# Kernel tuning notes

Measured on AMD Instinct MI355X. Metric: run time of the kernel, lower is better.

## Reference

```python
import jax, jax.numpy as jnp
import numpy as np

SR = 16000
NFFT = 512
NFILT = 64
FRAME_LEN = 400    # 0.025 * 16000
FRAME_STEP = 160   # 0.010 * 16000
NUM_FRAMES = 50000


def _mel_filterbanks():
    # python_speech_features get_filterbanks(nfilt=64, nfft=512, sr=16000, lowfreq=0, highfreq=sr/2)
    def hz2mel(hz):
        return 2595.0 * np.log10(1.0 + hz / 700.0)

    def mel2hz(m):
        return 700.0 * (10.0 ** (m / 2595.0) - 1.0)

    highfreq = SR / 2.0
    melpts = np.linspace(hz2mel(0.0), hz2mel(highfreq), NFILT + 2)
    bins = np.floor((NFFT + 1) * mel2hz(melpts) / SR)
    fb = np.zeros((NFILT, NFFT // 2 + 1), dtype=np.float64)
    for j in range(NFILT):
        for i in range(int(bins[j]), int(bins[j + 1])):
            fb[j, i] = (i - bins[j]) / (bins[j + 1] - bins[j])
        for i in range(int(bins[j + 1]), int(bins[j + 2])):
            fb[j, i] = (bins[j + 2] - i) / (bins[j + 2] - bins[j + 1])
    return fb.T.astype(np.float32)  # (257, nfilt) == filters.T in the original


def setup_inputs() -> dict:
    key = jax.random.key(0)
    audio_len = FRAME_LEN + (NUM_FRAMES - 1) * FRAME_STEP  # 8_000_240 -> exactly 50000 frames, zero pad
    x = jax.random.normal(key, (1, audio_len), dtype=jnp.float32)
    filters = jnp.asarray(_mel_filterbanks())
    return {"x": x, "filters": filters}


def reference(x, filters):
    # pre-emphasis
    x = jnp.concatenate([x[:, :1], x[:, 1:] - 0.97 * x[:, :-1]], axis=1)
    audio_len = x.shape[1]
    num_frames = (audio_len - FRAME_LEN) // FRAME_STEP + 1
    # vectorized framing (replaces the per-frame python slice/stack loop)
    idx = jnp.arange(num_frames)[:, None] * FRAME_STEP + jnp.arange(FRAME_LEN)[None, :]
    windowed = x[:, idx]                                     # (B, F, frame_len)
    r = jnp.fft.rfft(windowed, n=NFFT, axis=2)               # (B, F, nfft//2+1)
    power = (jnp.real(r) ** 2 + jnp.imag(r) ** 2) * (1.0 / NFFT)
    feat = jnp.einsum('bfk,kn->bfn', power, filters) + 1e-30  # (B, F, nfilt)
    # per-frame normalization over (batch, filters), matching reduce_mean/K.std on feat[:, i, :]
    m = jnp.mean(feat, axis=(0, 2), keepdims=True)
    s = jnp.std(feat, axis=(0, 2), keepdims=True)
    feat = (feat - m) / s
    return feat[..., None]                                   # (1, F, nfilt, 1)
```

## Files before the change

kernel.cpp:

```cpp
#include <hip/hip_runtime.h>
#include <math.h>

#define NFILT 64
#define FRAME_LEN 400
#define FRAME_STEP 160
#define WMAX 24
#define WSTRIDE 25
#define WAVES 4
#define NBLOCKS 1563
#define PWBINS 280

__global__ __launch_bounds__(256) void fbank_kernel(const float* __restrict__ x,
                                                    const float* __restrict__ filters,
                                                    float* __restrict__ out,
                                                    int num_frames) {
    __shared__ float wc_lds[NFILT * WSTRIDE];
    __shared__ int   lo_lds[NFILT];
    __shared__ float pw[WAVES][PWBINS * 2];

    const int t = threadIdx.x;
    const int l = t & 63;
    const int w = t >> 6;
    float* pwrow = pw[w];

    if (l < 2 * (PWBINS - 257)) pwrow[2 * 257 + l] = 0.0f;

    if (w == 0) {
        int lo = 257;
        for (int k = 0; k < 257; k++) {
            float fv = filters[k * NFILT + l];
            if (fv != 0.0f && lo == 257) lo = k;
        }
        if (lo > 256) lo = 256;
        lo_lds[l] = lo;
        for (int i = 0; i < WMAX; i++) {
            int k = lo + i;
            wc_lds[l * WSTRIDE + i] = (k <= 256) ? filters[k * NFILT + l] : 0.0f;
        }
    }

    const int rl = (int)(__brev((unsigned)l) >> 26);
    float cA[6], sA[6], sg[6];
#pragma unroll
    for (int j = 0; j < 6; j++) {
        const int d = 32 >> j;
        const int hi = l & d;
        float th = -2.0f * (float)M_PI * (float)(l & (d - 1)) / (float)(2 * d);
        cA[j] = hi ? cosf(th) : 1.0f;
        sA[j] = hi ? sinf(th) : 0.0f;
        sg[j] = hi ? -1.0f : 1.0f;
    }
    float br[8], bi[8];
    {
        float th = -2.0f * (float)M_PI * (float)rl * (1.0f / 512.0f);
        float c1 = cosf(th), s1 = sinf(th);
        br[0] = 1.0f; bi[0] = 0.0f; br[1] = c1; bi[1] = s1;
#pragma unroll
        for (int r = 2; r < 8; r++) {
            float pr_ = br[r - 1], pi_ = bi[r - 1];
            br[r] = pr_ * c1 - pi_ * s1;
            bi[r] = pr_ * s1 + pi_ * c1;
        }
    }
    const int Lp = (int)(__brev((unsigned)((64 - rl) & 63)) >> 26);

    __syncthreads();
    const int lo = lo_lds[l];

    const int gw = blockIdx.x * WAVES + w;
    const int totw = gridDim.x * WAVES;
    const int npairs = (num_frames + 1) >> 1;

    for (int pair = gw; pair < npairs; pair += totw) {
        const long fa = 2L * pair;
        const bool hasb = (fa + 1) < num_frames;
        const long ba = fa * FRAME_STEP;
        const long bb = ba + FRAME_STEP;

        float vr[8], vi[8];
        {
            float a0=0,a1=0,a2=0,a3=0,a4=0,a5=0,a6=0,a7=0;
            if (l < 50) {
                const float4* p4 = reinterpret_cast<const float4*>(x + ba + 8 * l);
                float4 A = p4[0], B = p4[1];
                a0=A.x; a1=A.y; a2=A.z; a3=A.w; a4=B.x; a5=B.y; a6=B.z; a7=B.w;
            }
            float ev = x[ba > 0 ? ba - 1 : 0];
            float edge = (ba > 0) ? ev : 0.0f;
            float prev = __shfl_up(a7, 1, 64);
            if (l == 0) prev = edge;
            vr[0] = (l < 50) ? fmaf(-0.97f, prev, a0) : 0.0f;
            vr[1] = (l < 50) ? fmaf(-0.97f, a0, a1) : 0.0f;
            vr[2] = (l < 50) ? fmaf(-0.97f, a1, a2) : 0.0f;
            vr[3] = (l < 50) ? fmaf(-0.97f, a2, a3) : 0.0f;
            vr[4] = (l < 50) ? fmaf(-0.97f, a3, a4) : 0.0f;
            vr[5] = (l < 50) ? fmaf(-0.97f, a4, a5) : 0.0f;
            vr[6] = (l < 50) ? fmaf(-0.97f, a5, a6) : 0.0f;
            vr[7] = (l < 50) ? fmaf(-0.97f, a6, a7) : 0.0f;
        }
        {
            float b0=0,b1=0,b2=0,b3=0,b4=0,b5=0,b6=0,b7=0;
            if (hasb && l < 50) {
                const float4* p4 = reinterpret_cast<const float4*>(x + bb + 8 * l);
                float4 A = p4[0], B = p4[1];
                b0=A.x; b1=A.y; b2=A.z; b3=A.w; b4=B.x; b5=B.y; b6=B.z; b7=B.w;
            }
            float edge = hasb ? x[bb - 1] : 0.0f;
            float prev = __shfl_up(b7, 1, 64);
            if (l == 0) prev = edge;
            vi[0] = (l < 50) ? fmaf(-0.97f, prev, b0) : 0.0f;
            vi[1] = (l < 50) ? fmaf(-0.97f, b0, b1) : 0.0f;
            vi[2] = (l < 50) ? fmaf(-0.97f, b1, b2) : 0.0f;
            vi[3] = (l < 50) ? fmaf(-0.97f, b2, b3) : 0.0f;
            vi[4] = (l < 50) ? fmaf(-0.97f, b3, b4) : 0.0f;
            vi[5] = (l < 50) ? fmaf(-0.97f, b4, b5) : 0.0f;
            vi[6] = (l < 50) ? fmaf(-0.97f, b5, b6) : 0.0f;
            vi[7] = (l < 50) ? fmaf(-0.97f, b6, b7) : 0.0f;
        }

#pragma unroll
        for (int j = 0; j < 6; j++) {
            const int d = 32 >> j;
            const float c = cA[j], s = sA[j], g = sg[j];
#pragma unroll
            for (int r = 0; r < 8; r++) {
                float pr = __shfl_xor(vr[r], d, 64);
                float pi = __shfl_xor(vi[r], d, 64);
                float tr = fmaf(g, vr[r], pr);
                float ti = fmaf(g, vi[r], pi);
                vr[r] = tr * c - ti * s;
                vi[r] = tr * s + ti * c;
            }
        }

#pragma unroll
        for (int r = 1; r < 8; r++) {
            float tr = vr[r], ti = vi[r];
            vr[r] = tr * br[r] - ti * bi[r];
            vi[r] = tr * bi[r] + ti * br[r];
        }

        const float RH = 0.70710678118654752f;
        {
            float t0r=vr[0]+vr[4], t0i=vi[0]+vi[4];
            float d0r=vr[0]-vr[4], d0i=vi[0]-vi[4];
            float t1r=vr[1]+vr[5], t1i=vi[1]+vi[5];
            float d1r=vr[1]-vr[5], d1i=vi[1]-vi[5];
            float t2r=vr[2]+vr[6], t2i=vi[2]+vi[6];
            float d2r=vr[2]-vr[6], d2i=vi[2]-vi[6];
            float t3r=vr[3]+vr[7], t3i=vi[3]+vi[7];
            float d3r=vr[3]-vr[7], d3i=vi[3]-vi[7];
            vr[0]=t0r; vi[0]=t0i; vr[1]=t1r; vi[1]=t1i;
            vr[2]=t2r; vi[2]=t2i; vr[3]=t3r; vi[3]=t3i;
            vr[4]=d0r;                 vi[4]=d0i;
            vr[5]=(d1r+d1i)*RH;        vi[5]=(d1i-d1r)*RH;
            vr[6]=d2i;                 vi[6]=-d2r;
            vr[7]=(d3i-d3r)*RH;        vi[7]=-(d3r+d3i)*RH;
        }
        {
            float t0r=vr[0]+vr[2], t0i=vi[0]+vi[2];
            float d0r=vr[0]-vr[2], d0i=vi[0]-vi[2];
            float t1r=vr[1]+vr[3], t1i=vi[1]+vi[3];
            float d1r=vr[1]-vr[3], d1i=vi[1]-vi[3];
            vr[0]=t0r; vi[0]=t0i; vr[1]=t1r; vi[1]=t1i;
            vr[2]=d0r; vi[2]=d0i; vr[3]=d1i; vi[3]=-d1r;
            float t4r=vr[4]+vr[6], t4i=vi[4]+vi[6];
            float d4r=vr[4]-vr[6], d4i=vi[4]-vi[6];
            float t5r=vr[5]+vr[7], t5i=vi[5]+vi[7];
            float d5r=vr[5]-vr[7], d5i=vi[5]-vi[7];
            vr[4]=t4r; vi[4]=t4i; vr[5]=t5r; vi[5]=t5i;
            vr[6]=d4r; vi[6]=d4i; vr[7]=d5i; vi[7]=-d5r;
        }
        {
            float t0r=vr[0]+vr[1], t0i=vi[0]+vi[1];
            float d0r=vr[0]-vr[1], d0i=vi[0]-vi[1];
            vr[0]=t0r; vi[0]=t0i; vr[1]=d0r; vi[1]=d0i;
            float t2r=vr[2]+vr[3], t2i=vi[2]+vi[3];
            float d2r=vr[2]-vr[3], d2i=vi[2]-vi[3];
            vr[2]=t2r; vi[2]=t2i; vr[3]=d2r; vi[3]=d2i;
            float t4r=vr[4]+vr[5], t4i=vi[4]+vi[5];
            float d4r=vr[4]-vr[5], d4i=vi[4]-vi[5];
            vr[4]=t4r; vi[4]=t4i; vr[5]=d4r; vi[5]=d4i;
            float t6r=vr[6]+vr[7], t6i=vi[6]+vi[7];
            float d6r=vr[6]-vr[7], d6i=vi[6]-vi[7];
            vr[6]=t6r; vi[6]=t6i; vr[7]=d6r; vi[7]=d6i;
        }

        float c0r = __shfl(vr[7], Lp, 64), c0i = __shfl(vi[7], Lp, 64);
        float c1r = __shfl(vr[3], Lp, 64), c1i = __shfl(vi[3], Lp, 64);
        float c2r = __shfl(vr[5], Lp, 64), c2i = __shfl(vi[5], Lp, 64);
        float c3r = __shfl(vr[1], Lp, 64), c3i = __shfl(vi[1], Lp, 64);
        if (l == 0) {
            c0r = vr[0]; c0i = vi[0];
            c1r = vr[7]; c1i = vi[7];
            c2r = vr[3]; c2i = vi[3];
            c3r = vr[5]; c3i = vi[5];
        }

        const float S4 = (1.0f / 512.0f) * 0.25f;
        {
            float zr = vr[0], zi = vi[0];
            float e1 = zr + c0r, e2 = zi - c0i, o1 = zi + c0i, o2 = c0r - zr;
            float2 pq = make_float2((e1*e1 + e2*e2) * S4, (o1*o1 + o2*o2) * S4);
            *reinterpret_cast<float2*>(&pwrow[2 * rl]) = pq;
        }
        {
            float zr = vr[4], zi = vi[4];
            float e1 = zr + c1r, e2 = zi - c1i, o1 = zi + c1i, o2 = c1r - zr;
            float2 pq = make_float2((e1*e1 + e2*e2) * S4, (o1*o1 + o2*o2) * S4);
            *reinterpret_cast<float2*>(&pwrow[2 * (rl + 64)]) = pq;
        }
        {
            float zr = vr[2], zi = vi[2];
            float e1 = zr + c2r, e2 = zi - c2i, o1 = zi + c2i, o2 = c2r - zr;
            float2 pq = make_float2((e1*e1 + e2*e2) * S4, (o1*o1 + o2*o2) * S4);
            *reinterpret_cast<float2*>(&pwrow[2 * (rl + 128)]) = pq;
        }
        {
            float zr = vr[6], zi = vi[6];
            float e1 = zr + c3r, e2 = zi - c3i, o1 = zi + c3i, o2 = c3r - zr;
            float2 pq = make_float2((e1*e1 + e2*e2) * S4, (o1*o1 + o2*o2) * S4);
            *reinterpret_cast<float2*>(&pwrow[2 * (rl + 192)]) = pq;
        }
        if (l == 0) {
            pwrow[512] = vr[1] * vr[1] * (1.0f / 512.0f);
            pwrow[513] = vi[1] * vi[1] * (1.0f / 512.0f);
        }

        asm volatile("s_waitcnt lgkmcnt(0)" ::: "memory");

        float acca = 1e-30f, accb = 1e-30f;
#pragma unroll
        for (int i = 0; i < WMAX; i++) {
            float wv = wc_lds[l * WSTRIDE + i];
            float2 pq = *reinterpret_cast<const float2*>(&pwrow[2 * (lo + i)]);
            acca = fmaf(wv, pq.x, acca);
            accb = fmaf(wv, pq.y, accb);
        }

        float sa = acca, sb = accb;
#pragma unroll
        for (int mk = 1; mk < 64; mk <<= 1) {
            sa += __shfl_xor(sa, mk, 64);
            sb += __shfl_xor(sb, mk, 64);
        }
        const float ma = sa * (1.0f / 64.0f), mb = sb * (1.0f / 64.0f);
        const float da = acca - ma, db = accb - mb;
        float va = da * da, vb = db * db;
#pragma unroll
        for (int mk = 1; mk < 64; mk <<= 1) {
            va += __shfl_xor(va, mk, 64);
            vb += __shfl_xor(vb, mk, 64);
        }
        out[fa * NFILT + l] = da / sqrtf(va * (1.0f / 64.0f));
        if (hasb)
            out[(fa + 1) * NFILT + l] = db / sqrtf(vb * (1.0f / 64.0f));
    }
}

extern "C" void kernel_launch(void* const* d_in, const int* in_sizes, int n_in,
                              void* d_out, int out_size, void* d_ws, size_t ws_size,
                              hipStream_t stream) {
    (void)d_ws; (void)ws_size; (void)n_in; (void)in_sizes;
    const float* x = (const float*)d_in[0];
    const float* filters = (const float*)d_in[1];
    float* out = (float*)d_out;
    const int num_frames = out_size / NFILT;
    fbank_kernel<<<NBLOCKS, 256, 0, stream>>>(x, filters, out, num_frames);
}
```

Baseline: 102.5 us.

## Process two frame-pairs per wave iteration with double power buffers

```diff
diff --git a/kernel.cpp b/kernel.cpp
--- a/kernel.cpp
+++ b/kernel.cpp
@@ -7,32 +7,184 @@
 #define WMAX 24
 #define WSTRIDE 25
 #define WAVES 4
-#define NBLOCKS 1563
+#define NBLOCKS 1024
 #define PWBINS 280
 
-__global__ __launch_bounds__(256) void fbank_kernel(const float* __restrict__ x,
-                                                    const float* __restrict__ filters,
-                                                    float* __restrict__ out,
-                                                    int num_frames) {
+__device__ __forceinline__ void load_pre(const float* __restrict__ x, long base,
+                                         int l, bool valid, float (&v)[8]) {
+    float a0=0,a1=0,a2=0,a3=0,a4=0,a5=0,a6=0,a7=0;
+    if (valid && l < 50) {
+        const float4* p4 = reinterpret_cast<const float4*>(x + base + 8 * l);
+        float4 A = p4[0], B = p4[1];
+        a0=A.x; a1=A.y; a2=A.z; a3=A.w; a4=B.x; a5=B.y; a6=B.z; a7=B.w;
+    }
+    float edge = 0.0f;
+    if (valid && base > 0) edge = x[base - 1];
+    float prev = __shfl_up(a7, 1, 64);
+    if (l == 0) prev = edge;
+    const bool act = valid && (l < 50);
+    v[0] = act ? fmaf(-0.97f, prev, a0) : 0.0f;
+    v[1] = act ? fmaf(-0.97f, a0, a1) : 0.0f;
+    v[2] = act ? fmaf(-0.97f, a1, a2) : 0.0f;
+    v[3] = act ? fmaf(-0.97f, a2, a3) : 0.0f;
+    v[4] = act ? fmaf(-0.97f, a3, a4) : 0.0f;
+    v[5] = act ? fmaf(-0.97f, a4, a5) : 0.0f;
+    v[6] = act ? fmaf(-0.97f, a5, a6) : 0.0f;
+    v[7] = act ? fmaf(-0.97f, a6, a7) : 0.0f;
+}
+
+__device__ __forceinline__ void fft512(float (&vr)[8], float (&vi)[8],
+                                       const float (&cA)[6], const float (&sA)[6],
+                                       const float (&sg)[6],
+                                       const float (&br)[8], const float (&bi)[8]) {
+#pragma unroll
+    for (int j = 0; j < 6; j++) {
+        const int d = 32 >> j;
+        const float c = cA[j], s = sA[j], g = sg[j];
+#pragma unroll
+        for (int r = 0; r < 8; r++) {
+            float pr = __shfl_xor(vr[r], d, 64);
+            float pi = __shfl_xor(vi[r], d, 64);
+            float tr = fmaf(g, vr[r], pr);
+            float ti = fmaf(g, vi[r], pi);
+            vr[r] = tr * c - ti * s;
+            vi[r] = tr * s + ti * c;
+        }
+    }
+#pragma unroll
+    for (int r = 1; r < 8; r++) {
+        float tr = vr[r], ti = vi[r];
+        vr[r] = tr * br[r] - ti * bi[r];
+        vi[r] = tr * bi[r] + ti * br[r];
+    }
+    const float RH = 0.70710678118654752f;
+    {
+        float t0r=vr[0]+vr[4], t0i=vi[0]+vi[4];
+        float d0r=vr[0]-vr[4], d0i=vi[0]-vi[4];
+        float t1r=vr[1]+vr[5], t1i=vi[1]+vi[5];
+        float d1r=vr[1]-vr[5], d1i=vi[1]-vi[5];
+        float t2r=vr[2]+vr[6], t2i=vi[2]+vi[6];
+        float d2r=vr[2]-vr[6], d2i=vi[2]-vi[6];
+        float t3r=vr[3]+vr[7], t3i=vi[3]+vi[7];
+        float d3r=vr[3]-vr[7], d3i=vi[3]-vi[7];
+        vr[0]=t0r; vi[0]=t0i; vr[1]=t1r; vi[1]=t1i;
+        vr[2]=t2r; vi[2]=t2i; vr[3]=t3r; vi[3]=t3i;
+        vr[4]=d0r;                 vi[4]=d0i;
+        vr[5]=(d1r+d1i)*RH;        vi[5]=(d1i-d1r)*RH;
+        vr[6]=d2i;                 vi[6]=-d2r;
+        vr[7]=(d3i-d3r)*RH;        vi[7]=-(d3r+d3i)*RH;
+    }
+    {
+        float t0r=vr[0]+vr[2], t0i=vi[0]+vi[2];
+        float d0r=vr[0]-vr[2], d0i=vi[0]-vi[2];
+        float t1r=vr[1]+vr[3], t1i=vi[1]+vi[3];
+        float d1r=vr[1]-vr[3], d1i=vi[1]-vi[3];
+        vr[0]=t0r; vi[0]=t0i; vr[1]=t1r; vi[1]=t1i;
+        vr[2]=d0r; vi[2]=d0i; vr[3]=d1i; vi[3]=-d1r;
+        float t4r=vr[4]+vr[6], t4i=vi[4]+vi[6];
+        float d4r=vr[4]-vr[6], d4i=vi[4]-vi[6];
+        float t5r=vr[5]+vr[7], t5i=vi[5]+vi[7];
+        float d5r=vr[5]-vr[7], d5i=vi[5]-vi[7];
+        vr[4]=t4r; vi[4]=t4i; vr[5]=t5r; vi[5]=t5i;
+        vr[6]=d4r; vi[6]=d4i; vr[7]=d5i; vi[7]=-d5r;
+    }
+    {
+        float t0r=vr[0]+vr[1], t0i=vi[0]+vi[1];
+        float d0r=vr[0]-vr[1], d0i=vi[0]-vi[1];
+        vr[0]=t0r; vi[0]=t0i; vr[1]=d0r; vi[1]=d0i;
+        float t2r=vr[2]+vr[3], t2i=vi[2]+vi[3];
+        float d2r=vr[2]-vr[3], d2i=vi[2]-vi[3];
+        vr[2]=t2r; vi[2]=t2i; vr[3]=d2r; vi[3]=d2i;
+        float t4r=vr[4]+vr[5], t4i=vi[4]+vi[5];
+        float d4r=vr[4]-vr[5], d4i=vi[4]-vi[5];
+        vr[4]=t4r; vi[4]=t4i; vr[5]=d4r; vi[5]=d4i;
+        float t6r=vr[6]+vr[7], t6i=vi[6]+vi[7];
+        float d6r=vr[6]-vr[7], d6i=vi[6]-vi[7];
+        vr[6]=t6r; vi[6]=t6i; vr[7]=d6r; vi[7]=d6i;
+    }
+}
+
+__device__ __forceinline__ void untangle_power(const float (&vr)[8], const float (&vi)[8],
+                                               int l, int rl, int Lp,
+                                               float* __restrict__ pwrow) {
+    float c0r = __shfl(vr[7], Lp, 64), c0i = __shfl(vi[7], Lp, 64);
+    float c1r = __shfl(vr[3], Lp, 64), c1i = __shfl(vi[3], Lp, 64);
+    float c2r = __shfl(vr[5], Lp, 64), c2i = __shfl(vi[5], Lp, 64);
+    float c3r = __shfl(vr[1], Lp, 64), c3i = __shfl(vi[1], Lp, 64);
+    if (l == 0) {
+        c0r = vr[0]; c0i = vi[0];
+        c1r = vr[7]; c1i = vi[7];
+        c2r = vr[3]; c2i = vi[3];
+        c3r = vr[5]; c3i = vi[5];
+    }
+    const float S4 = (1.0f / 512.0f) * 0.25f;
+    {
+        float zr = vr[0], zi = vi[0];
+        float e1 = zr + c0r, e2 = zi - c0i, o1 = zi + c0i, o2 = c0r - zr;
+        *reinterpret_cast<float2*>(&pwrow[2 * rl]) =
+            make_float2((e1*e1 + e2*e2) * S4, (o1*o1 + o2*o2) * S4);
+    }
+    {
+        float zr = vr[4], zi = vi[4];
+        float e1 = zr + c1r, e2 = zi - c1i, o1 = zi + c1i, o2 = c1r - zr;
+        *reinterpret_cast<float2*>(&pwrow[2 * (rl + 64)]) =
+            make_float2((e1*e1 + e2*e2) * S4, (o1*o1 + o2*o2) * S4);
+    }
+    {
+        float zr = vr[2], zi = vi[2];
+        float e1 = zr + c2r, e2 = zi - c2i, o1 = zi + c2i, o2 = c2r - zr;
+        *reinterpret_cast<float2*>(&pwrow[2 * (rl + 128)]) =
+            make_float2((e1*e1 + e2*e2) * S4, (o1*o1 + o2*o2) * S4);
+    }
+    {
+        float zr = vr[6], zi = vi[6];
+        float e1 = zr + c3r, e2 = zi - c3i, o1 = zi + c3i, o2 = c3r - zr;
+        *reinterpret_cast<float2*>(&pwrow[2 * (rl + 192)]) =
+            make_float2((e1*e1 + e2*e2) * S4, (o1*o1 + o2*o2) * S4);
+    }
+    if (l == 0) {
+        pwrow[512] = vr[1] * vr[1] * (1.0f / 512.0f);
+        pwrow[513] = vi[1] * vi[1] * (1.0f / 512.0f);
+    }
+}
+
+__global__ __launch_bounds__(256, 4) void fbank_kernel(const float* __restrict__ x,
+                                                       const float* __restrict__ filters,
+                                                       float* __restrict__ out,
+                                                       int num_frames) {
     __shared__ float wc_lds[NFILT * WSTRIDE];
     __shared__ int   lo_lds[NFILT];
-    __shared__ float pw[WAVES][PWBINS * 2];
+    __shared__ float pw[WAVES][2][PWBINS * 2];
 
     const int t = threadIdx.x;
     const int l = t & 63;
     const int w = t >> 6;
-    float* pwrow = pw[w];
-
-    if (l < 2 * (PWBINS - 257)) pwrow[2 * 257 + l] = 0.0f;
+    float* pwA = pw[w][0];
+    float* pwB = pw[w][1];
+
+    if (l < 2 * (PWBINS - 257)) {
+        pwA[2 * 257 + l] = 0.0f;
+        pwB[2 * 257 + l] = 0.0f;
+    }
 
     if (w == 0) {
         int lo = 257;
-        for (int k = 0; k < 257; k++) {
-            float fv = filters[k * NFILT + l];
-            if (fv != 0.0f && lo == 257) lo = k;
+#pragma unroll 4
+        for (int k0 = 0; k0 < 264; k0 += 8) {
+            float fv[8];
+#pragma unroll
+            for (int i = 0; i < 8; i++) {
+                int k = k0 + i;
+                fv[i] = (k < 257) ? filters[k * NFILT + l] : 0.0f;
+            }
+#pragma unroll
+            for (int i = 0; i < 8; i++) {
+                if (fv[i] != 0.0f && lo == 257) lo = k0 + i;
+            }
         }
         if (lo > 256) lo = 256;
         lo_lds[l] = lo;
+#pragma unroll
         for (int i = 0; i < WMAX; i++) {
             int k = lo + i;
             wc_lds[l * WSTRIDE + i] = (k <= 256) ? filters[k * NFILT + l] : 0.0f;
@@ -68,193 +220,70 @@
     const int lo = lo_lds[l];
 
     const int gw = blockIdx.x * WAVES + w;
-    const int totw = gridDim.x * WAVES;
+    const int totw = NBLOCKS * WAVES;
     const int npairs = (num_frames + 1) >> 1;
 
-    for (int pair = gw; pair < npairs; pair += totw) {
-        const long fa = 2L * pair;
-        const bool hasb = (fa + 1) < num_frames;
-        const long ba = fa * FRAME_STEP;
-        const long bb = ba + FRAME_STEP;
-
-        float vr[8], vi[8];
-        {
-            float a0=0,a1=0,a2=0,a3=0,a4=0,a5=0,a6=0,a7=0;
-            if (l < 50) {
-                const float4* p4 = reinterpret_cast<const float4*>(x + ba + 8 * l);
-                float4 A = p4[0], B = p4[1];
-                a0=A.x; a1=A.y; a2=A.z; a3=A.w; a4=B.x; a5=B.y; a6=B.z; a7=B.w;
-            }
-            float ev = x[ba > 0 ? ba - 1 : 0];
-            float edge = (ba > 0) ? ev : 0.0f;
-            float prev = __shfl_up(a7, 1, 64);
-            if (l == 0) prev = edge;
-            vr[0] = (l < 50) ? fmaf(-0.97f, prev, a0) : 0.0f;
-            vr[1] = (l < 50) ? fmaf(-0.97f, a0, a1) : 0.0f;
-            vr[2] = (l < 50) ? fmaf(-0.97f, a1, a2) : 0.0f;
-            vr[3] = (l < 50) ? fmaf(-0.97f, a2, a3) : 0.0f;
-            vr[4] = (l < 50) ? fmaf(-0.97f, a3, a4) : 0.0f;
-            vr[5] = (l < 50) ? fmaf(-0.97f, a4, a5) : 0.0f;
-            vr[6] = (l < 50) ? fmaf(-0.97f, a5, a6) : 0.0f;
-            vr[7] = (l < 50) ? fmaf(-0.97f, a6, a7) : 0.0f;
-        }
-        {
-            float b0=0,b1=0,b2=0,b3=0,b4=0,b5=0,b6=0,b7=0;
-            if (hasb && l < 50) {
-                const float4* p4 = reinterpret_cast<const float4*>(x + bb + 8 * l);
-                float4 A = p4[0], B = p4[1];
-                b0=A.x; b1=A.y; b2=A.z; b3=A.w; b4=B.x; b5=B.y; b6=B.z; b7=B.w;
-            }
-            float edge = hasb ? x[bb - 1] : 0.0f;
-            float prev = __shfl_up(b7, 1, 64);
-            if (l == 0) prev = edge;
-            vi[0] = (l < 50) ? fmaf(-0.97f, prev, b0) : 0.0f;
-            vi[1] = (l < 50) ? fmaf(-0.97f, b0, b1) : 0.0f;
-            vi[2] = (l < 50) ? fmaf(-0.97f, b1, b2) : 0.0f;
-            vi[3] = (l < 50) ? fmaf(-0.97f, b2, b3) : 0.0f;
-            vi[4] = (l < 50) ? fmaf(-0.97f, b3, b4) : 0.0f;
-            vi[5] = (l < 50) ? fmaf(-0.97f, b4, b5) : 0.0f;
-            vi[6] = (l < 50) ? fmaf(-0.97f, b5, b6) : 0.0f;
-            vi[7] = (l < 50) ? fmaf(-0.97f, b6, b7) : 0.0f;
-        }
-
-#pragma unroll
-        for (int j = 0; j < 6; j++) {
-            const int d = 32 >> j;
-            const float c = cA[j], s = sA[j], g = sg[j];
-#pragma unroll
-            for (int r = 0; r < 8; r++) {
-                float pr = __shfl_xor(vr[r], d, 64);
-                float pi = __shfl_xor(vi[r], d, 64);
-                float tr = fmaf(g, vr[r], pr);
-                float ti = fmaf(g, vi[r], pi);
-                vr[r] = tr * c - ti * s;
-                vi[r] = tr * s + ti * c;
-            }
-        }
-
-#pragma unroll
-        for (int r = 1; r < 8; r++) {
-            float tr = vr[r], ti = vi[r];
-            vr[r] = tr * br[r] - ti * bi[r];
-            vi[r] = tr * bi[r] + ti * br[r];
-        }
-
-        const float RH = 0.70710678118654752f;
-        {
-            float t0r=vr[0]+vr[4], t0i=vi[0]+vi[4];
-            float d0r=vr[0]-vr[4], d0i=vi[0]-vi[4];
-            float t1r=vr[1]+vr[5], t1i=vi[1]+vi[5];
-            float d1r=vr[1]-vr[5], d1i=vi[1]-vi[5];
-            float t2r=vr[2]+vr[6], t2i=vi[2]+vi[6];
-            float d2r=vr[2]-vr[6], d2i=vi[2]-vi[6];
-            float t3r=vr[3]+vr[7], t3i=vi[3]+vi[7];
-            float d3r=vr[3]-vr[7], d3i=vi[3]-vi[7];
-            vr[0]=t0r; vi[0]=t0i; vr[1]=t1r; vi[1]=t1i;
-            vr[2]=t2r; vi[2]=t2i; vr[3]=t3r; vi[3]=t3i;
-            vr[4]=d0r;                 vi[4]=d0i;
-            vr[5]=(d1r+d1i)*RH;        vi[5]=(d1i-d1r)*RH;
-            vr[6]=d2i;                 vi[6]=-d2r;
-            vr[7]=(d3i-d3r)*RH;        vi[7]=-(d3r+d3i)*RH;
-        }
-        {
-            float t0r=vr[0]+vr[2], t0i=vi[0]+vi[2];
-            float d0r=vr[0]-vr[2], d0i=vi[0]-vi[2];
-            float t1r=vr[1]+vr[3], t1i=vi[1]+vi[3];
-            float d1r=vr[1]-vr[3], d1i=vi[1]-vi[3];
-            vr[0]=t0r; vi[0]=t0i; vr[1]=t1r; vi[1]=t1i;
-            vr[2]=d0r; vi[2]=d0i; vr[3]=d1i; vi[3]=-d1r;
-            float t4r=vr[4]+vr[6], t4i=vi[4]+vi[6];
-            float d4r=vr[4]-vr[6], d4i=vi[4]-vi[6];
-            float t5r=vr[5]+vr[7], t5i=vi[5]+vi[7];
-            float d5r=vr[5]-vr[7], d5i=vi[5]-vi[7];
-            vr[4]=t4r; vi[4]=t4i; vr[5]=t5r; vi[5]=t5i;
-            vr[6]=d4r; vi[6]=d4i; vr[7]=d5i; vi[7]=-d5r;
-        }
-        {
-            float t0r=vr[0]+vr[1], t0i=vi[0]+vi[1];
-            float d0r=vr[0]-vr[1], d0i=vi[0]-vi[1];
-            vr[0]=t0r; vi[0]=t0i; vr[1]=d0r; vi[1]=d0i;
-            float t2r=vr[2]+vr[3], t2i=vi[2]+vi[3];
-            float d2r=vr[2]-vr[3], d2i=vi[2]-vi[3];
-            vr[2]=t2r; vi[2]=t2i; vr[3]=d2r; vi[3]=d2i;
-            float t4r=vr[4]+vr[5], t4i=vi[4]+vi[5];
-            float d4r=vr[4]-vr[5], d4i=vi[4]-vi[5];
-            vr[4]=t4r; vi[4]=t4i; vr[5]=d4r; vi[5]=d4i;
-            float t6r=vr[6]+vr[7], t6i=vi[6]+vi[7];
-            float d6r=vr[6]-vr[7], d6i=vi[6]-vi[7];
-            vr[6]=t6r; vi[6]=t6i; vr[7]=d6r; vi[7]=d6i;
-        }
-
-        float c0r = __shfl(vr[7], Lp, 64), c0i = __shfl(vi[7], Lp, 64);
-        float c1r = __shfl(vr[3], Lp, 64), c1i = __shfl(vi[3], Lp, 64);
-        float c2r = __shfl(vr[5], Lp, 64), c2i = __shfl(vi[5], Lp, 64);
-        float c3r = __shfl(vr[1], Lp, 64), c3i = __shfl(vi[1], Lp, 64);
-        if (l == 0) {
-            c0r = vr[0]; c0i = vi[0];
-            c1r = vr[7]; c1i = vi[7];
-            c2r = vr[3]; c2i = vi[3];
-            c3r = vr[5]; c3i = vi[5];
-        }
-
-        const float S4 = (1.0f / 512.0f) * 0.25f;
-        {
-            float zr = vr[0], zi = vi[0];
-            float e1 = zr + c0r, e2 = zi - c0i, o1 = zi + c0i, o2 = c0r - zr;
-            float2 pq = make_float2((e1*e1 + e2*e2) * S4, (o1*o1 + o2*o2) * S4);
-            *reinterpret_cast<float2*>(&pwrow[2 * rl]) = pq;
-        }
-        {
-            float zr = vr[4], zi = vi[4];
-            float e1 = zr + c1r, e2 = zi - c1i, o1 = zi + c1i, o2 = c1r - zr;
-            float2 pq = make_float2((e1*e1 + e2*e2) * S4, (o1*o1 + o2*o2) * S4);
-            *reinterpret_cast<float2*>(&pwrow[2 * (rl + 64)]) = pq;
-        }
-        {
-            float zr = vr[2], zi = vi[2];
-            float e1 = zr + c2r, e2 = zi - c2i, o1 = zi + c2i, o2 = c2r - zr;
-            float2 pq = make_float2((e1*e1 + e2*e2) * S4, (o1*o1 + o2*o2) * S4);
-            *reinterpret_cast<float2*>(&pwrow[2 * (rl + 128)]) = pq;
-        }
-        {
-            float zr = vr[6], zi = vi[6];
-            float e1 = zr + c3r, e2 = zi - c3i, o1 = zi + c3i, o2 = c3r - zr;
-            float2 pq = make_float2((e1*e1 + e2*e2) * S4, (o1*o1 + o2*o2) * S4);
-            *reinterpret_cast<float2*>(&pwrow[2 * (rl + 192)]) = pq;
-        }
-        if (l == 0) {
-            pwrow[512] = vr[1] * vr[1] * (1.0f / 512.0f);
-            pwrow[513] = vi[1] * vi[1] * (1.0f / 512.0f);
-        }
+    for (int p0 = gw; p0 < npairs; p0 += 2 * totw) {
+        const int p1 = p0 + totw;
+        const bool v1 = (p1 < npairs);
+        const int p1c = v1 ? p1 : p0;
+
+        const long fA = 2L * p0;
+        const long fB = 2L * p1c;
+        const bool hasbA = (fA + 1) < num_frames;
+        const bool hasbB = (fB + 1) < num_frames;
+
+        float vrA[8], viA[8], vrB[8], viB[8];
+        load_pre(x, fA * FRAME_STEP, l, true, vrA);
+        load_pre(x, (fA + 1) * FRAME_STEP, l, hasbA, viA);
+        load_pre(x, fB * FRAME_STEP, l, true, vrB);
+        load_pre(x, (fB + 1) * FRAME_STEP, l, hasbB, viB);
+
+        fft512(vrA, viA, cA, sA, sg, br, bi);
+        fft512(vrB, viB, cA, sA, sg, br, bi);
+
+        untangle_power(vrA, viA, l, rl, Lp, pwA);
+        untangle_power(vrB, viB, l, rl, Lp, pwB);
 
         asm volatile("s_waitcnt lgkmcnt(0)" ::: "memory");
 
-        float acca = 1e-30f, accb = 1e-30f;
+        float ac0 = 1e-30f, ac1 = 1e-30f, ac2 = 1e-30f, ac3 = 1e-30f;
 #pragma unroll
         for (int i = 0; i < WMAX; i++) {
             float wv = wc_lds[l * WSTRIDE + i];
-            float2 pq = *reinterpret_cast<const float2*>(&pwrow[2 * (lo + i)]);
-            acca = fmaf(wv, pq.x, acca);
-            accb = fmaf(wv, pq.y, accb);
-        }
-
-        float sa = acca, sb = accb;
+            float2 pA = *reinterpret_cast<const float2*>(&pwA[2 * (lo + i)]);
+            float2 pB = *reinterpret_cast<const float2*>(&pwB[2 * (lo + i)]);
+            ac0 = fmaf(wv, pA.x, ac0);
+            ac1 = fmaf(wv, pA.y, ac1);
+            ac2 = fmaf(wv, pB.x, ac2);
+            ac3 = fmaf(wv, pB.y, ac3);
+        }
+
+        float s0 = ac0, s1 = ac1, s2 = ac2, s3 = ac3;
 #pragma unroll
         for (int mk = 1; mk < 64; mk <<= 1) {
-            sa += __shfl_xor(sa, mk, 64);
-            sb += __shfl_xor(sb, mk, 64);
-        }
-        const float ma = sa * (1.0f / 64.0f), mb = sb * (1.0f / 64.0f);
-        const float da = acca - ma, db = accb - mb;
-        float va = da * da, vb = db * db;
+            s0 += __shfl_xor(s0, mk, 64);
+            s1 += __shfl_xor(s1, mk, 64);
+            s2 += __shfl_xor(s2, mk, 64);
+            s3 += __shfl_xor(s3, mk, 64);
+        }
+        const float m0 = s0 * (1.0f/64.0f), m1 = s1 * (1.0f/64.0f);
+        const float m2 = s2 * (1.0f/64.0f), m3 = s3 * (1.0f/64.0f);
+        const float d0 = ac0 - m0, d1 = ac1 - m1, d2 = ac2 - m2, d3 = ac3 - m3;
+        float q0 = d0*d0, q1 = d1*d1, q2 = d2*d2, q3 = d3*d3;
 #pragma unroll
         for (int mk = 1; mk < 64; mk <<= 1) {
-            va += __shfl_xor(va, mk, 64);
-            vb += __shfl_xor(vb, mk, 64);
-        }
-        out[fa * NFILT + l] = da / sqrtf(va * (1.0f / 64.0f));
-        if (hasb)
-            out[(fa + 1) * NFILT + l] = db / sqrtf(vb * (1.0f / 64.0f));
+            q0 += __shfl_xor(q0, mk, 64);
+            q1 += __shfl_xor(q1, mk, 64);
+            q2 += __shfl_xor(q2, mk, 64);
+            q3 += __shfl_xor(q3, mk, 64);
+        }
+        out[fA * NFILT + l] = d0 / sqrtf(q0 * (1.0f/64.0f));
+        if (hasbA) out[(fA + 1) * NFILT + l] = d1 / sqrtf(q1 * (1.0f/64.0f));
+        if (v1) {
+            out[fB * NFILT + l] = d2 / sqrtf(q2 * (1.0f/64.0f));
+            if (hasbB) out[(fB + 1) * NFILT + l] = d3 / sqrtf(q3 * (1.0f/64.0f));
+        }
     }
 }
 
```

Measured after the change: 134.7 us. +31.4%, slower.
